# Kernel tuning notes

Measured on AMD Instinct MI355X. Metric: run time of the kernel, lower is better.

The kernel has to match this reference:

```python
import jax, jax.numpy as jnp
import numpy as np

K = 3  # kernel_size

def setup_inputs() -> dict:
    key = jax.random.key(0)
    k1, k2, k3 = jax.random.split(key, 3)
    B, T, G, F, O = 4, 512, 129, 96, 96
    x = jax.random.normal(k1, (B, T, G, F), dtype=jnp.float32)
    # kaiming_uniform_(a=sqrt(5)) -> bound = sqrt(6/((1+5)*fan_in)) = 1/sqrt(fan_in), fan_in = F*K
    fan_in = F * K
    wb = 1.0 / np.sqrt(fan_in)
    weight = jax.random.uniform(k2, (G, O, F, K), dtype=jnp.float32, minval=-wb, maxval=wb)
    bias = jax.random.uniform(k3, (G, O), dtype=jnp.float32, minval=-wb, maxval=wb)
    return {"x": x, "weight": weight, "bias": bias}

def reference(x, weight, bias):
    # x: [B, T, G, F]; weight: [G, O, F, K]; bias: [G, O]
    B, T, G, F = x.shape
    pad = K // 2
    xp = jnp.pad(x, ((0, 0), (pad, pad), (0, 0), (0, 0)))  # [B, T+2p, G, F]
    # gather K shifted views -> [B, T, G, F, K] (same windows as unfold with padding K//2)
    xw = jnp.stack([xp[:, k:k + T] for k in range(K)], axis=-1)
    out = jnp.einsum('btgfk,gofk->btgo', xw, weight)
    out = out + bias  # broadcast [G, O] over [B, T, G, O]
    return out
```

## Files before the change

### kernel.cpp

```cpp
#include <hip/hip_runtime.h>
#include <hip/hip_bf16.h>

typedef unsigned short ushort_t;
typedef __attribute__((ext_vector_type(8))) short short8;
typedef __attribute__((ext_vector_type(4))) float floatx4;

#define G_   129
#define F_   96
#define O_   96
#define T_   512
#define KD   288
#define LDB  296
#define SROW 40
#define SLAB (36 * SROW)

__device__ __forceinline__ unsigned f2bf(float f) {
    unsigned u = __builtin_bit_cast(unsigned, f);
    u += 0x7FFFu + ((u >> 16) & 1u);
    return u >> 16;
}
__device__ __forceinline__ unsigned pk2(float a, float b) {
    return f2bf(a) | (f2bf(b) << 16);
}

__global__ void wt_permute(const float* __restrict__ w, ushort_t* __restrict__ wt) {
    int i = blockIdx.x * 256 + threadIdx.x;
    const int total = G_ * O_ * KD;
    if (i >= total) return;
    int base = i / KD;
    int kd = i - base * KD;
    int kk = kd / F_;
    int f  = kd - kk * F_;
    wt[i] = (ushort_t)f2bf(w[base * KD + f * 3 + kk]);
}

__global__ __launch_bounds__(512, 4) void conv_mfma(
    const float* __restrict__ x, const ushort_t* __restrict__ wt,
    const float* __restrict__ bias, float* __restrict__ out)
{
    __shared__ __align__(16) ushort_t Wl[O_ * LDB];
    __shared__ __align__(16) ushort_t Xs[8 * SLAB];

    const int g    = blockIdx.y;
    const int m0   = blockIdx.x * 256;
    const int tid  = threadIdx.x;
    const int wave = tid >> 6;
    const int lane = tid & 63;
    const int ln   = lane & 15;
    const int q    = lane >> 4;

    {
        const ushort_t* src = wt + (size_t)g * (O_ * KD);
        for (int idx = tid; idx < O_ * 36; idx += 512) {
            int o = idx / 36;
            int s = idx - o * 36;
            *(short8*)&Wl[o * LDB + s * 8] = *(const short8*)&src[o * KD + s * 8];
        }
    }
    __syncthreads();

    const int m0r = m0 + wave * 32;
    const int b   = m0r >> 9;
    const int tb  = m0r & 511;

    const float* tp[5];
    int  laddr[5];
    bool wr[5], vld[5];
    #pragma unroll
    for (int i = 0; i < 5; ++i) {
        int task = i * 64 + lane;
        int row = task >> 3;
        int seg = task & 7;
        int tl = tb + row - 1;
        wr[i]  = row < 34;
        vld[i] = wr[i] && ((unsigned)tl < (unsigned)T_);
        int tc = tl < 0 ? 0 : (tl > T_ - 1 ? T_ - 1 : tl);
        tp[i] = x + ((size_t)((b * T_ + tc) * G_ + g) * F_ + seg * 4);
        laddr[i] = wave * SLAB + row * SROW + seg * 4;
    }

    auto issueX = [&](int fb, floatx4* v) {
        #pragma unroll
        for (int i = 0; i < 5; ++i)
            v[i] = *(const floatx4*)(tp[i] + fb * 32);
    };
    auto writeX = [&](const floatx4* v) {
        #pragma unroll
        for (int i = 0; i < 5; ++i) {
            if (wr[i]) {
                unsigned lo = pk2(v[i][0], v[i][1]);
                unsigned hi = pk2(v[i][2], v[i][3]);
                if (!vld[i]) { lo = 0u; hi = 0u; }
                uint2 d; d.x = lo; d.y = hi;
                *(uint2*)&Xs[laddr[i]] = d;
            }
        }
    };

    floatx4 acc[2][6];
    #pragma unroll
    for (int s = 0; s < 2; ++s)
        #pragma unroll
        for (int nt = 0; nt < 6; ++nt)
            acc[s][nt] = (floatx4){0.f, 0.f, 0.f, 0.f};

    floatx4 cur[5], nxt[5];
    issueX(0, cur);

    #pragma unroll
    for (int fb = 0; fb < 3; ++fb) {
        if (fb < 2) issueX(fb + 1, nxt);
        writeX(cur);

        #pragma unroll
        for (int kk = 0; kk < 3; ++kk) {
            const short8 a0 = *(const short8*)&Xs[wave * SLAB + (ln + kk) * SROW + q * 8];
            const short8 a1 = *(const short8*)&Xs[wave * SLAB + (16 + ln + kk) * SROW + q * 8];
            const int c32 = (kk * 3 + fb) * 32;
            #pragma unroll
            for (int nt = 0; nt < 6; ++nt) {
                const short8 bb = *(const short8*)&Wl[(nt * 16 + ln) * LDB + c32 + q * 8];
                acc[0][nt] = __builtin_amdgcn_mfma_f32_16x16x32_bf16(a0, bb, acc[0][nt], 0, 0, 0);
                acc[1][nt] = __builtin_amdgcn_mfma_f32_16x16x32_bf16(a1, bb, acc[1][nt], 0, 0, 0);
            }
        }
        #pragma unroll
        for (int i = 0; i < 5; ++i) cur[i] = nxt[i];
    }

    #pragma unroll
    for (int s = 0; s < 2; ++s) {
        int mbase = m0 + wave * 32 + s * 16 + q * 4;
        #pragma unroll
        for (int nt = 0; nt < 6; ++nt) {
            int o = nt * 16 + ln;
            float bv = bias[g * O_ + o];
            #pragma unroll
            for (int r = 0; r < 4; ++r) {
                int m = mbase + r;
                out[(size_t)(m * G_ + g) * O_ + o] = acc[s][nt][r] + bv;
            }
        }
    }
}

extern "C" void kernel_launch(void* const* d_in, const int* in_sizes, int n_in,
                              void* d_out, int out_size, void* d_ws, size_t ws_size,
                              hipStream_t stream) {
    const float* x    = (const float*)d_in[0];
    const float* w    = (const float*)d_in[1];
    const float* bias = (const float*)d_in[2];
    float* out = (float*)d_out;
    ushort_t* wt = (ushort_t*)d_ws;

    const int total_w = G_ * O_ * KD;
    wt_permute<<<dim3((total_w + 255) / 256), dim3(256), 0, stream>>>(w, wt);

    dim3 grid(2048 / 256, G_);
    conv_mfma<<<grid, dim3(512), 0, stream>>>(x, wt, bias, out);
}
```

Before: 217.4 us.

## Fuse weight permute/bf16 conversion into conv kernel and prefetch X before weight load

Removes the separate wt_permute kernel launch and instead has each conv block read the fp32 weights for its group directly, converting to bf16 and permuting into the (k,f) LDS layout in-kernel. The first X tile load is issued before the weight staging so its latency overlaps the weight conversion, and the bias load is hoisted before the main loop. The cost is that each of the 8 blocks per group redundantly reads and converts fp32 weights (twice the bytes of bf16), adding global traffic and ALU work per block.

```diff
diff --git a/kernel.cpp b/kernel.cpp
--- a/kernel.cpp
+++ b/kernel.cpp
@@ -1,5 +1,4 @@
 #include <hip/hip_runtime.h>
-#include <hip/hip_bf16.h>
 
 typedef unsigned short ushort_t;
 typedef __attribute__((ext_vector_type(8))) short short8;
@@ -23,19 +22,8 @@
     return f2bf(a) | (f2bf(b) << 16);
 }
 
-__global__ void wt_permute(const float* __restrict__ w, ushort_t* __restrict__ wt) {
-    int i = blockIdx.x * 256 + threadIdx.x;
-    const int total = G_ * O_ * KD;
-    if (i >= total) return;
-    int base = i / KD;
-    int kd = i - base * KD;
-    int kk = kd / F_;
-    int f  = kd - kk * F_;
-    wt[i] = (ushort_t)f2bf(w[base * KD + f * 3 + kk]);
-}
-
 __global__ __launch_bounds__(512, 4) void conv_mfma(
-    const float* __restrict__ x, const ushort_t* __restrict__ wt,
+    const float* __restrict__ x, const float* __restrict__ w,
     const float* __restrict__ bias, float* __restrict__ out)
 {
     __shared__ __align__(16) ushort_t Wl[O_ * LDB];
@@ -48,16 +36,6 @@
     const int lane = tid & 63;
     const int ln   = lane & 15;
     const int q    = lane >> 4;
-
-    {
-        const ushort_t* src = wt + (size_t)g * (O_ * KD);
-        for (int idx = tid; idx < O_ * 36; idx += 512) {
-            int o = idx / 36;
-            int s = idx - o * 36;
-            *(short8*)&Wl[o * LDB + s * 8] = *(const short8*)&src[o * KD + s * 8];
-        }
-    }
-    __syncthreads();
 
     const int m0r = m0 + wave * 32;
     const int b   = m0r >> 9;
@@ -97,6 +75,39 @@
         }
     };
 
+    floatx4 va[5], vb[5];
+    issueX(0, va);
+
+    {
+        const float* wg = w + (size_t)g * (O_ * KD);
+        #pragma unroll
+        for (int i = 0; i < 5; ++i) {
+            int task = i * 512 + tid;
+            if (task < 2304) {
+                int o = task / 24;
+                int u = task - o * 24;
+                const float* p = wg + o * KD + u * 12;
+                float4 A = *(const float4*)(p);
+                float4 B = *(const float4*)(p + 4);
+                float4 C = *(const float4*)(p + 8);
+                int base = o * LDB + u * 4;
+                uint2 d0, d1, d2;
+                d0.x = pk2(A.x, A.w);  d0.y = pk2(B.z, C.y);
+                d1.x = pk2(A.y, B.x);  d1.y = pk2(B.w, C.z);
+                d2.x = pk2(A.z, B.y);  d2.y = pk2(C.x, C.w);
+                *(uint2*)&Wl[base]       = d0;
+                *(uint2*)&Wl[base +  96] = d1;
+                *(uint2*)&Wl[base + 192] = d2;
+            }
+        }
+    }
+
+    float bv[6];
+    #pragma unroll
+    for (int nt = 0; nt < 6; ++nt) bv[nt] = bias[g * O_ + nt * 16 + ln];
+
+    __syncthreads();
+
     floatx4 acc[2][6];
     #pragma unroll
     for (int s = 0; s < 2; ++s)
@@ -104,14 +115,7 @@
         for (int nt = 0; nt < 6; ++nt)
             acc[s][nt] = (floatx4){0.f, 0.f, 0.f, 0.f};
 
-    floatx4 cur[5], nxt[5];
-    issueX(0, cur);
-
-    #pragma unroll
-    for (int fb = 0; fb < 3; ++fb) {
-        if (fb < 2) issueX(fb + 1, nxt);
-        writeX(cur);
-
+    auto compute = [&](int fb) {
         #pragma unroll
         for (int kk = 0; kk < 3; ++kk) {
             const short8 a0 = *(const short8*)&Xs[wave * SLAB + (ln + kk) * SROW + q * 8];
@@ -119,14 +123,21 @@
             const int c32 = (kk * 3 + fb) * 32;
             #pragma unroll
             for (int nt = 0; nt < 6; ++nt) {
-                const short8 bb = *(const short8*)&Wl[(nt * 16 + ln) * LDB + c32 + q * 8];
-                acc[0][nt] = __builtin_amdgcn_mfma_f32_16x16x32_bf16(a0, bb, acc[0][nt], 0, 0, 0);
-                acc[1][nt] = __builtin_amdgcn_mfma_f32_16x16x32_bf16(a1, bb, acc[1][nt], 0, 0, 0);
+                const short8 bbv = *(const short8*)&Wl[(nt * 16 + ln) * LDB + c32 + q * 8];
+                acc[0][nt] = __builtin_amdgcn_mfma_f32_16x16x32_bf16(a0, bbv, acc[0][nt], 0, 0, 0);
+                acc[1][nt] = __builtin_amdgcn_mfma_f32_16x16x32_bf16(a1, bbv, acc[1][nt], 0, 0, 0);
             }
         }
-        #pragma unroll
-        for (int i = 0; i < 5; ++i) cur[i] = nxt[i];
-    }
+    };
+
+    issueX(1, vb);
+    writeX(va);
+    compute(0);
+    issueX(2, va);
+    writeX(vb);
+    compute(1);
+    writeX(va);
+    compute(2);
 
     #pragma unroll
     for (int s = 0; s < 2; ++s) {
@@ -134,11 +145,10 @@
         #pragma unroll
         for (int nt = 0; nt < 6; ++nt) {
             int o = nt * 16 + ln;
-            float bv = bias[g * O_ + o];
             #pragma unroll
             for (int r = 0; r < 4; ++r) {
                 int m = mbase + r;
-                out[(size_t)(m * G_ + g) * O_ + o] = acc[s][nt][r] + bv;
+                out[(size_t)(m * G_ + g) * O_ + o] = acc[s][nt][r] + bv[nt];
             }
         }
     }
@@ -151,11 +161,6 @@
     const float* w    = (const float*)d_in[1];
     const float* bias = (const float*)d_in[2];
     float* out = (float*)d_out;
-    ushort_t* wt = (ushort_t*)d_ws;
-
-    const int total_w = G_ * O_ * KD;
-    wt_permute<<<dim3((total_w + 255) / 256), dim3(256), 0, stream>>>(w, wt);
-
     dim3 grid(2048 / 256, G_);
-    conv_mfma<<<grid, dim3(512), 0, stream>>>(x, wt, bias, out);
+    conv_mfma<<<grid, dim3(512), 0, stream>>>(x, w, bias, out);
 }
```

New measurement: 214.2 us. Within noise of the previous version (-1.5%).
